# Kernel tuning notes

Hardware: AMD Instinct MI355X
Metric: run time of the kernel (lower is better)

## Reference

```python
import jax, jax.numpy as jnp
import numpy as np

N, K, E = 20000, 4, 320000
IN_DIM, H_IN, D = 1024, 256, 128
GATE_IN = 2 * D + 1  # [h || m || logdeg]
GATE_H = 128         # max(d_out, 32)
TEMP = 0.6
M_CLAMP = 20.0


def _init(key, shape, fan_in):
    return jax.random.normal(key, shape, dtype=jnp.float32) / np.sqrt(fan_in)


def setup_inputs() -> dict:
    key = jax.random.key(0)
    ks = jax.random.split(key, 24)
    inp = {}
    inp['X'] = jax.random.normal(ks[0], (N, IN_DIM), dtype=jnp.float32)
    inp['rows'] = jax.random.randint(ks[1], (K, E), 0, N, dtype=jnp.int32)
    inp['cols'] = jax.random.randint(ks[2], (K, E), 0, N, dtype=jnp.int32)
    inp['mask'] = jnp.ones((N, K), dtype=jnp.float32)
    inp['logdeg'] = jax.random.uniform(ks[3], (N, K), dtype=jnp.float32) * 3.0
    # lin_in: 3-layer MLP 1024 -> 256 -> 256 -> 128, each + ReLU
    inp['W_in0'] = _init(ks[4], (IN_DIM, H_IN), IN_DIM); inp['b_in0'] = jnp.zeros((H_IN,), jnp.float32)
    inp['W_in1'] = _init(ks[5], (H_IN, H_IN), H_IN);     inp['b_in1'] = jnp.zeros((H_IN,), jnp.float32)
    inp['W_in2'] = _init(ks[6], (H_IN, D), H_IN);        inp['b_in2'] = jnp.zeros((D,), jnp.float32)
    # block 0
    inp['Wmsg0'] = _init(ks[7], (D, D), D)
    inp['Wg1_0'] = _init(ks[8], (GATE_IN, GATE_H), GATE_IN); inp['bg1_0'] = jnp.zeros((GATE_H,), jnp.float32)
    inp['Wg2_0'] = _init(ks[9], (GATE_H, 1), GATE_H);        inp['bg2_0'] = jnp.zeros((1,), jnp.float32)
    # block 1
    inp['Wmsg1'] = _init(ks[10], (D, D), D)
    inp['Wg1_1'] = _init(ks[11], (GATE_IN, GATE_H), GATE_IN); inp['bg1_1'] = jnp.zeros((GATE_H,), jnp.float32)
    inp['Wg2_1'] = _init(ks[12], (GATE_H, 1), GATE_H);        inp['bg2_1'] = jnp.zeros((1,), jnp.float32)
    # head
    inp['Wh1'] = _init(ks[13], (D, D), D); inp['bh1'] = jnp.zeros((D,), jnp.float32)
    inp['Wh2'] = _init(ks[14], (D, 1), D); inp['bh2'] = jnp.zeros((1,), jnp.float32)
    return inp


def reference(X, rows, cols, mask, logdeg,
              W_in0, b_in0, W_in1, b_in1, W_in2, b_in2,
              Wmsg0, Wg1_0, bg1_0, Wg2_0, bg2_0,
              Wmsg1, Wg1_1, bg1_1, Wg2_1, bg2_1,
              Wh1, bh1, Wh2, bh2):
    relu = jax.nn.relu
    # input encoder (eval mode: dropout / featdrop are identity)
    H = relu(relu(relu(X @ W_in0 + b_in0) @ W_in1 + b_in1) @ W_in2 + b_in2)

    def pairnorm(x):
        x = x - x.mean(axis=0, keepdims=True)
        mean_norm = jnp.sqrt(jnp.mean(jnp.sum(x * x, axis=1))) + 1e-6
        return x / mean_norm

    def block(H, Wmsg, Wg1, bg1, Wg2, bg2):
        Z = H @ Wmsg  # [N, D]
        def prop(r, c):  # sparse A_k @ Z with binary adjacency: out[r] += Z[c]
            return jax.ops.segment_sum(Z[c], r, num_segments=N)
        M = jnp.transpose(jax.vmap(prop)(rows, cols), (1, 0, 2))  # [N, K, D]
        M = jnp.clip(M, -M_CLAMP, M_CLAMP)
        H_rep = jnp.broadcast_to(H[:, None, :], (N, K, H.shape[1]))
        gate_in = jnp.concatenate([H_rep, M, logdeg[:, :, None]], axis=2)  # [N, K, 2D+1]
        scores = (relu(gate_in @ Wg1 + bg1) @ Wg2 + bg2)[..., 0]  # [N, K]
        alpha = jax.nn.softmax(scores / TEMP, axis=1)
        alpha = alpha * mask
        alpha = alpha / jnp.maximum(alpha.sum(axis=1, keepdims=True), 1e-12)
        alpha = jnp.maximum(alpha, 1e-8)
        alpha = alpha / jnp.maximum(alpha.sum(axis=1, keepdims=True), 1e-12)
        fused = jnp.einsum('nk,nkd->nd', alpha, M)
        return fused, alpha

    fused0, a0 = block(H, Wmsg0, Wg1_0, bg1_0, Wg2_0, bg2_0)
    H = relu(pairnorm(fused0 + H))
    fused1, a1 = block(H, Wmsg1, Wg1_1, bg1_1, Wg2_1, bg2_1)
    H = relu(pairnorm(fused1 + H))

    h = relu(relu(H) @ Wh1 + bh1)
    logits = (h @ Wh2 + bh2)[:, 0]  # [N]
    return logits, jnp.stack([a0, a1], axis=0)
```

## Files before the change

kernel.cpp:

```cpp
#include <hip/hip_runtime.h>
#include <hip/hip_bf16.h>

#define N_NODES 20000
#define KADJ 4
#define NEDGE 320000
#define ETOTAL (KADJ * NEDGE)
#define IN_DIM_ 1024
#define H_IN_ 256
#define DDIM 128
#define GATE_H_ 128
#define TEMP_ 0.6f
#define M_CLAMP_ 20.0f
#define CSR_TOTAL (KADJ * N_NODES)
#define NCOARSE 128
#define QPER (CSR_TOTAL / NCOARSE)
#define ESTRIDE 12288
#define TILE_A 4096
#define BINA_NB ((ETOTAL + TILE_A - 1) / TILE_A)
#define NB_CAST (N_NODES * IN_DIM_ / 8 / 256)
#define NB_TRANS 2560

typedef __attribute__((ext_vector_type(8))) short frag_ab;
typedef __attribute__((ext_vector_type(4))) float frag_cd;
typedef __attribute__((ext_vector_type(8))) unsigned short us8;

__device__ inline unsigned short f2bf(float f) {
    unsigned int u = __float_as_uint(f);
    u += 0x7FFFu + ((u >> 16) & 1);
    return (unsigned short)(u >> 16);
}
__device__ inline float bflo(unsigned int p) { return __uint_as_float(p << 16); }
__device__ inline float bfhi(unsigned int p) { return __uint_as_float(p & 0xffff0000u); }

__device__ __forceinline__ void gld16(const unsigned short* g, unsigned short* l) {
    __builtin_amdgcn_global_load_lds(
        (const __attribute__((address_space(1))) void*)g,
        (__attribute__((address_space(3))) void*)l, 16, 0, 0);
}

#define PIPE_WAIT_NEXT()  asm volatile("s_waitcnt vmcnt(5)" ::: "memory")
#define PIPE_WAIT_LAST()  asm volatile("s_waitcnt vmcnt(0)" ::: "memory")
#define PIPE_BAR()        __builtin_amdgcn_s_barrier()
#define PIPE_FENCE()      __builtin_amdgcn_sched_barrier(0)


struct TD { const float* src; unsigned short* dst; int K; int N; };
struct TD10 { TD d[10]; };

__global__ __launch_bounds__(256) void prep_kernel(
    const float* __restrict__ X, unsigned short* __restrict__ Xb,
    TD10 descs,
    const int* __restrict__ rows, const int* __restrict__ cols,
    int* __restrict__ bcnt, uint2* __restrict__ staging)
{
    __shared__ __align__(16) char sraw[2048 + TILE_A * 8];
    int bid = blockIdx.x;
    int tid = threadIdx.x;

    if (bid < NB_CAST) {
        int i = (bid * 256 + tid) * 8;
        float4 a = *(const float4*)(X + i), b = *(const float4*)(X + i + 4);
        us8 o;
        o[0] = f2bf(a.x); o[1] = f2bf(a.y); o[2] = f2bf(a.z); o[3] = f2bf(a.w);
        o[4] = f2bf(b.x); o[5] = f2bf(b.y); o[6] = f2bf(b.z); o[7] = f2bf(b.w);
        *(us8*)(Xb + i) = o;
        return;
    }
    if (bid < NB_CAST + NB_TRANS) {
        int b2 = bid - NB_CAST;
        TD t = descs.d[b2 >> 8];
        int rem = b2 & 255;
        int n0 = (rem & 7) * 32, k0 = (rem >> 3) * 32;
        if (n0 >= t.N || k0 >= t.K) return;
        float (*tile)[33] = (float(*)[33])sraw;
        int tx = tid & 31, ty4 = (tid >> 5) * 4;
#pragma unroll
        for (int i = 0; i < 4; i++)
            tile[ty4 + i][tx] = t.src[(size_t)(k0 + ty4 + i) * t.N + n0 + tx];
        __syncthreads();
#pragma unroll
        for (int i = 0; i < 4; i++)
            t.dst[(size_t)(n0 + ty4 + i) * t.K + k0 + tx] = f2bf(tile[tx][ty4 + i]);
        return;
    }
    int* hist  = (int*)sraw;
    int* hscan = hist + NCOARSE;
    int* lcur  = hscan + NCOARSE;
    int* gbase = lcur + NCOARSE;
    uint2* pairs = (uint2*)(sraw + 2048);

    int base = (bid - NB_CAST - NB_TRANS) * TILE_A;
    int cnt_t = min(TILE_A, ETOTAL - base);

    for (int i = tid; i < NCOARSE; i += 256) hist[i] = 0;
    __syncthreads();

    unsigned int q[16], c[16];
    bool valid[16];
#pragma unroll
    for (int i = 0; i < 16; i++) {
        int loc = i * 256 + tid;
        valid[i] = loc < cnt_t;
        if (valid[i]) {
            int e = base + loc;
            int k = e / NEDGE;
            unsigned int qq = (unsigned int)(k * N_NODES + rows[e]);
            q[i] = qq;
            c[i] = (unsigned int)cols[e];
            atomicAdd(&hist[qq / QPER], 1);
        }
    }
    __syncthreads();
    if (tid < NCOARSE) hscan[tid] = hist[tid];
    __syncthreads();
    for (int d = 1; d < NCOARSE; d <<= 1) {
        int v = (tid >= d && tid < NCOARSE) ? hscan[tid - d] : 0;
        __syncthreads();
        if (tid < NCOARSE) hscan[tid] += v;
        __syncthreads();
    }
    if (tid < NCOARSE) {
        int ex = hscan[tid] - hist[tid];
        hscan[tid] = ex;
        lcur[tid] = ex;
        gbase[tid] = hist[tid] ? (tid * ESTRIDE + atomicAdd(&bcnt[tid], hist[tid])) : 0;
    }
    __syncthreads();
#pragma unroll
    for (int i = 0; i < 16; i++) {
        if (valid[i]) {
            int b = q[i] / QPER;
            int p = atomicAdd(&lcur[b], 1);
            pairs[p] = make_uint2(q[i], c[i]);
        }
    }
    __syncthreads();
    for (int i = tid; i < cnt_t; i += 256) {
        uint2 pr = pairs[i];
        int b = pr.x / QPER;
        staging[gbase[b] + (i - hscan[b])] = pr;
    }
}

__global__ __launch_bounds__(256) void gemm_async_kernel(
    const unsigned short* __restrict__ A, const unsigned short* __restrict__ Bt,
    const float* __restrict__ bias, float* __restrict__ Cf, unsigned short* __restrict__ Cb,
    int M, int N, int K, int do_relu)
{
    __shared__ unsigned short sA[2][32 * 64];
    __shared__ unsigned short sB[2][128 * 64];
    int tid = threadIdx.x;
    int tileM = blockIdx.y * 32, tileN = blockIdx.x * 128;
    int w = tid >> 6, lane = tid & 63;
    int wr = (w & 1) * 16, wc = (w >> 1) * 64;
    int fm = lane & 15, fq = lane >> 4;
    int crow = lane >> 3;
    int gsw = (lane & 7) ^ crow;

    frag_cd acc[4] = {};

    auto stage = [&](int buf, int k0) {
        {
            int row = w * 8 + crow;
            int ar = min(tileM + row, M - 1);
            gld16(A + (size_t)ar * K + k0 + gsw * 8, &sA[buf][w * 512]);
        }
#pragma unroll
        for (int t = 0; t < 4; t++) {
            int chunk = w * 4 + t;
            int row = chunk * 8 + crow;
            gld16(Bt + (size_t)(tileN + row) * K + k0 + gsw * 8, &sB[buf][chunk * 512]);
        }
    };

    int nt = K >> 6;
    stage(0, 0);
    for (int t = 0; t < nt; t++) {
        int cur = t & 1;
        if (t + 1 < nt) { stage(cur ^ 1, (t + 1) << 6); PIPE_WAIT_NEXT(); }
        else            { PIPE_WAIT_LAST(); }
        PIPE_BAR();
        PIPE_FENCE();
#pragma unroll
        for (int s = 0; s < 2; s++) {
            int sw = ((s * 4 + fq) ^ (fm & 7)) * 8;
            frag_ab af = *(const frag_ab*)&sA[cur][(wr + fm) * 64 + sw];
#pragma unroll
            for (int j = 0; j < 4; j++) {
                frag_ab bf = *(const frag_ab*)&sB[cur][(wc + j * 16 + fm) * 64 + sw];
                acc[j] = __builtin_amdgcn_mfma_f32_16x16x32_bf16(af, bf, acc[j], 0, 0, 0);
            }
        }
        PIPE_FENCE();
        PIPE_BAR();
    }
    int row = tileM + wr + fq * 4;
#pragma unroll
    for (int r = 0; r < 4; r++) {
        if (row + r < M) {
#pragma unroll
            for (int j = 0; j < 4; j++) {
                int col = tileN + wc + j * 16 + fm;
                float v = acc[j][r];
                if (bias) v += bias[col];
                if (do_relu) v = fmaxf(v, 0.f);
                if (Cf) Cf[(size_t)(row + r) * N + col] = v;
                if (Cb) Cb[(size_t)(row + r) * N + col] = f2bf(v);
            }
        }
    }
}

__global__ __launch_bounds__(256) void zg_gemm_kernel(
    const unsigned short* __restrict__ A, const unsigned short* __restrict__ Bt,
    const float* __restrict__ bg1, unsigned short* __restrict__ Zb,
    float* __restrict__ GH, int M)
{
    __shared__ unsigned short sA[2][32 * 64];
    __shared__ unsigned short sB[2][128 * 64];
    int tid = threadIdx.x;
    int tileM = blockIdx.y * 32, tileN = blockIdx.x * 128;
    int w = tid >> 6, lane = tid & 63;
    int wr = (w & 1) * 16, wc = (w >> 1) * 64;
    int fm = lane & 15, fq = lane >> 4;
    int crow = lane >> 3;
    int gsw = (lane & 7) ^ crow;

    frag_cd acc[4] = {};

    auto stage = [&](int buf, int k0) {
        {
            int row = w * 8 + crow;
            int ar = min(tileM + row, M - 1);
            gld16(A + (size_t)ar * DDIM + k0 + gsw * 8, &sA[buf][w * 512]);
        }
#pragma unroll
        for (int t = 0; t < 4; t++) {
            int chunk = w * 4 + t;
            int row = chunk * 8 + crow;
            gld16(Bt + (size_t)(tileN + row) * DDIM + k0 + gsw * 8, &sB[buf][chunk * 512]);
        }
    };

    stage(0, 0);
#pragma unroll
    for (int t = 0; t < 2; t++) {
        int cur = t & 1;
        if (t == 0) { stage(1, 64); PIPE_WAIT_NEXT(); }
        else        { PIPE_WAIT_LAST(); }
        PIPE_BAR();
        PIPE_FENCE();
#pragma unroll
        for (int s = 0; s < 2; s++) {
            int sw = ((s * 4 + fq) ^ (fm & 7)) * 8;
            frag_ab af = *(const frag_ab*)&sA[cur][(wr + fm) * 64 + sw];
#pragma unroll
            for (int j = 0; j < 4; j++) {
                frag_ab bf = *(const frag_ab*)&sB[cur][(wc + j * 16 + fm) * 64 + sw];
                acc[j] = __builtin_amdgcn_mfma_f32_16x16x32_bf16(af, bf, acc[j], 0, 0, 0);
            }
        }
        PIPE_FENCE();
        PIPE_BAR();
    }
    int isZ = (blockIdx.x == 0);
    int row = tileM + wr + fq * 4;
#pragma unroll
    for (int r = 0; r < 4; r++) {
        if (row + r < M) {
#pragma unroll
            for (int j = 0; j < 4; j++) {
                int col = wc + j * 16 + fm;
                float v = acc[j][r];
                if (isZ) Zb[(size_t)(row + r) * DDIM + col] = f2bf(v);
                else     GH[(size_t)(row + r) * GATE_H_ + col] = v + bg1[col];
            }
        }
    }
}

__global__ __launch_bounds__(256) void head_gemm_kernel(
    const unsigned short* __restrict__ A, const unsigned short* __restrict__ Bt,
    const float* __restrict__ bh1, const float* __restrict__ Wh2,
    const float* __restrict__ bh2, float* __restrict__ logits, int M)
{
    __shared__ unsigned short sA[2][32 * 64];
    __shared__ unsigned short sB[2][128 * 64];
    __shared__ float sred[2][32];
    int tid = threadIdx.x;
    int tileM = blockIdx.x * 32;
    int w = tid >> 6, lane = tid & 63;
    int wr = (w & 1) * 16, wc = (w >> 1) * 64;
    int fm = lane & 15, fq = lane >> 4;
    int crow = lane >> 3;
    int gsw = (lane & 7) ^ crow;

    frag_cd acc[4] = {};

    auto stage = [&](int buf, int k0) {
        {
            int row = w * 8 + crow;
            int ar = min(tileM + row, M - 1);
            gld16(A + (size_t)ar * DDIM + k0 + gsw * 8, &sA[buf][w * 512]);
        }
#pragma unroll
        for (int t = 0; t < 4; t++) {
            int chunk = w * 4 + t;
            int row = chunk * 8 + crow;
            gld16(Bt + (size_t)row * DDIM + k0 + gsw * 8, &sB[buf][chunk * 512]);
        }
    };

    stage(0, 0);
#pragma unroll
    for (int t = 0; t < 2; t++) {
        int cur = t & 1;
        if (t == 0) { stage(1, 64); PIPE_WAIT_NEXT(); }
        else        { PIPE_WAIT_LAST(); }
        PIPE_BAR();
        PIPE_FENCE();
#pragma unroll
        for (int s = 0; s < 2; s++) {
            int sw = ((s * 4 + fq) ^ (fm & 7)) * 8;
            frag_ab af = *(const frag_ab*)&sA[cur][(wr + fm) * 64 + sw];
#pragma unroll
            for (int j = 0; j < 4; j++) {
                frag_ab bf = *(const frag_ab*)&sB[cur][(wc + j * 16 + fm) * 64 + sw];
                acc[j] = __builtin_amdgcn_mfma_f32_16x16x32_bf16(af, bf, acc[j], 0, 0, 0);
            }
        }
        PIPE_FENCE();
        PIPE_BAR();
    }
    float wv[4], bh[4];
#pragma unroll
    for (int j = 0; j < 4; j++) {
        int c = wc + j * 16 + fm;
        wv[j] = Wh2[c];
        bh[j] = bh1[c];
    }
    float part[4];
#pragma unroll
    for (int r = 0; r < 4; r++) {
        float p = 0.f;
#pragma unroll
        for (int j = 0; j < 4; j++) {
            float v = fmaxf(acc[j][r] + bh[j], 0.f);
            p += v * wv[j];
        }
        part[r] = p;
    }
#pragma unroll
    for (int m = 1; m < 16; m <<= 1)
#pragma unroll
        for (int r = 0; r < 4; r++)
            part[r] += __shfl_xor(part[r], m, 64);
    if (fm == 0) {
#pragma unroll
        for (int r = 0; r < 4; r++)
            sred[w >> 1][wr + fq * 4 + r] = part[r];
    }
    __syncthreads();
    if (tid < 32 && tileM + tid < M)
        logits[tileM + tid] = sred[0][tid] + sred[1][tid] + bh2[0];
}

__global__ __launch_bounds__(256) void gate_fuse_kernel(
    const unsigned short* __restrict__ Mb, const unsigned short* __restrict__ Bt,
    const float* __restrict__ GH, const float* __restrict__ logdeg,
    const float* __restrict__ wld, const float* __restrict__ Wg2,
    const float* __restrict__ bg2, const float* __restrict__ mask,
    const float* __restrict__ H, float* __restrict__ Y,
    float* __restrict__ alpha_out, float* __restrict__ red)
{
    __shared__ unsigned short sA[2][32 * 64];
    __shared__ unsigned short sB[2][128 * 64];
    __shared__ float sred[2][32];
    __shared__ float sc_al[64];
    __shared__ float sx[256], sy[256], sqs[256];
    int tid = threadIdx.x;
    int tile0 = blockIdx.x * 32;
    int node0 = blockIdx.x * 8;
    int w = tid >> 6, lane = tid & 63;
    int wr = (w & 1) * 16, wc = (w >> 1) * 64;
    int fm = lane & 15, fq = lane >> 4;
    int crow = lane >> 3;
    int gsw = (lane & 7) ^ crow;

    frag_cd acc[4] = {};

    auto stage = [&](int buf, int k0) {
        {
            int row = w * 8 + crow;
            gld16(Mb + (size_t)(tile0 + row) * DDIM + k0 + gsw * 8, &sA[buf][w * 512]);
        }
#pragma unroll
        for (int t = 0; t < 4; t++) {
            int chunk = w * 4 + t;
            int row = chunk * 8 + crow;
            gld16(Bt + (size_t)row * DDIM + k0 + gsw * 8, &sB[buf][chunk * 512]);
        }
    };

    stage(0, 0);
#pragma unroll
    for (int t = 0; t < 2; t++) {
        int cur = t & 1;
        if (t == 0) { stage(1, 64); PIPE_WAIT_NEXT(); }
        else        { PIPE_WAIT_LAST(); }
        PIPE_BAR();
        PIPE_FENCE();
#pragma unroll
        for (int s = 0; s < 2; s++) {
            int sw = ((s * 4 + fq) ^ (fm & 7)) * 8;
            frag_ab af = *(const frag_ab*)&sA[cur][(wr + fm) * 64 + sw];
#pragma unroll
            for (int j = 0; j < 4; j++) {
                frag_ab bf = *(const frag_ab*)&sB[cur][(wc + j * 16 + fm) * 64 + sw];
                acc[j] = __builtin_amdgcn_mfma_f32_16x16x32_bf16(af, bf, acc[j], 0, 0, 0);
            }
        }
        PIPE_FENCE();
        PIPE_BAR();
    }
    float wg2v[4], wldv[4];
#pragma unroll
    for (int j = 0; j < 4; j++) {
        int c = wc + j * 16 + fm;
        wg2v[j] = Wg2[c];
        wldv[j] = wld[c];
    }
    float part[4];
#pragma unroll
    for (int r = 0; r < 4; r++) {
        int q = tile0 + wr + fq * 4 + r;
        int n = q >> 2;
        float ld = logdeg[q];
        float p = 0.f;
#pragma unroll
        for (int j = 0; j < 4; j++) {
            int c = wc + j * 16 + fm;
            float v = acc[j][r] + GH[(size_t)n * GATE_H_ + c] + ld * wldv[j];
            p += fmaxf(v, 0.f) * wg2v[j];
        }
        part[r] = p;
    }
#pragma unroll
    for (int m = 1; m < 16; m <<= 1)
#pragma unroll
        for (int r = 0; r < 4; r++)
            part[r] += __shfl_xor(part[r], m, 64);
    if (fm == 0) {
#pragma unroll
        for (int r = 0; r < 4; r++)
            sred[w >> 1][wr + fq * 4 + r] = part[r];
    }
    __syncthreads();
    if (tid < 32) sc_al[tid] = sred[0][tid] + sred[1][tid] + bg2[0];
    __syncthreads();
    if (tid < 8) {
        int n = node0 + tid;
        float a[KADJ];
        float mx = -1e30f;
#pragma unroll
        for (int k = 0; k < KADJ; k++) {
            a[k] = sc_al[tid * 4 + k] * (1.0f / TEMP_);
            mx = fmaxf(mx, a[k]);
        }
        float sum = 0.f;
#pragma unroll
        for (int k = 0; k < KADJ; k++) { a[k] = expf(a[k] - mx); sum += a[k]; }
#pragma unroll
        for (int k = 0; k < KADJ; k++) a[k] = (a[k] / sum) * mask[(size_t)n * KADJ + k];
        float s2 = 0.f;
#pragma unroll
        for (int k = 0; k < KADJ; k++) s2 += a[k];
        float inv = 1.f / fmaxf(s2, 1e-12f);
#pragma unroll
        for (int k = 0; k < KADJ; k++) a[k] = fmaxf(a[k] * inv, 1e-8f);
        s2 = 0.f;
#pragma unroll
        for (int k = 0; k < KADJ; k++) s2 += a[k];
        inv = 1.f / fmaxf(s2, 1e-12f);
#pragma unroll
        for (int k = 0; k < KADJ; k++) sc_al[32 + tid * 4 + k] = a[k] * inv;
    }
    __syncthreads();
    if (tid < 32) alpha_out[tile0 + tid] = sc_al[32 + tid];
    float csx = 0.f, csy = 0.f, sq = 0.f;
    int j = tid & 63, dd = j * 2;
#pragma unroll
    for (int it = 0; it < 2; it++) {
        int nl = (tid >> 6) + it * 4;
        int n = node0 + nl;
        const float* alp = &sc_al[32 + nl * 4];
        float2 h = *(const float2*)(H + (size_t)n * DDIM + dd);
        float yx = h.x, yy = h.y;
#pragma unroll
        for (int k = 0; k < KADJ; k++) {
            unsigned int u = *(const unsigned int*)(Mb + ((size_t)n * KADJ + k) * DDIM + dd);
            yx += alp[k] * bflo(u);
            yy += alp[k] * bfhi(u);
        }
        *(float2*)(Y + (size_t)n * DDIM + dd) = make_float2(yx, yy);
        csx += yx; csy += yy;
        sq += yx * yx + yy * yy;
    }
    sx[tid] = csx; sy[tid] = csy; sqs[tid] = sq;
    __syncthreads();
    int st = (blockIdx.x & 7) * 132;
    if (tid < 64) {
        float ax = sx[tid] + sx[tid + 64] + sx[tid + 128] + sx[tid + 192];
        float ay = sy[tid] + sy[tid + 64] + sy[tid + 128] + sy[tid + 192];
        atomicAdd(&red[st + tid * 2], ax);
        atomicAdd(&red[st + tid * 2 + 1], ay);
    }
    for (int s = 128; s > 0; s >>= 1) {
        if (tid < s) sqs[tid] += sqs[tid + s];
        __syncthreads();
    }
    if (tid == 0) atomicAdd(&red[st + 128], sqs[0]);
}

__global__ __launch_bounds__(256) void binB2_kernel(
    const uint2* __restrict__ staging, const int* __restrict__ bcnt,
    int* __restrict__ offs, int* __restrict__ ends, int* __restrict__ edst)
{
    __shared__ int cntS[QPER], sofs[QPER], lcur[QPER];
    __shared__ int psum[256];
    int tid = threadIdx.x, b = blockIdx.x;
    int q0 = b * QPER, base = b * ESTRIDE;
    int fill = bcnt[b];
    for (int i = tid; i < QPER; i += 256) cntS[i] = 0;
    __syncthreads();
    for (int i = tid; i < fill; i += 256)
        atomicAdd(&cntS[staging[base + i].x - q0], 1);
    __syncthreads();
    const int CH = 3;
    int lo = tid * CH, hi = min(lo + CH, QPER);
    int s = 0;
    for (int i = lo; i < hi; i++) s += cntS[i];
    psum[tid] = s;
    __syncthreads();
    for (int d = 1; d < 256; d <<= 1) {
        int v = (tid >= d) ? psum[tid - d] : 0;
        __syncthreads();
        psum[tid] += v;
        __syncthreads();
    }
    int run = (tid == 0) ? 0 : psum[tid - 1];
    for (int i = lo; i < hi; i++) {
        sofs[i] = run;
        lcur[i] = run;
        run += cntS[i];
    }
    __syncthreads();
    for (int i = tid; i < QPER; i += 256) {
        offs[q0 + i] = base + sofs[i];
        ends[q0 + i] = base + sofs[i] + cntS[i];
    }
    for (int i = tid; i < fill; i += 256) {
        uint2 p = staging[base + i];
        int pos = atomicAdd(&lcur[p.x - q0], 1);
        edst[base + pos] = (int)p.y;
    }
}

__global__ __launch_bounds__(256) void gather_kernel(
    const int* __restrict__ offs, const int* __restrict__ ends,
    const int* __restrict__ edst,
    const unsigned short* __restrict__ Zb, unsigned short* __restrict__ Mb)
{
    int q = blockIdx.x * 4 + (threadIdx.x >> 6);
    int lane = threadIdx.x & 63;
    int qw = lane >> 4;
    int l = lane & 15;
    int k = q / N_NODES;
    int r = q - k * N_NODES;
    int start = offs[q];
    int end = ends[q];

    float a0 = 0.f, a1 = 0.f, a2 = 0.f, a3 = 0.f;
    float a4 = 0.f, a5 = 0.f, a6 = 0.f, a7 = 0.f;

#define ACC8(P) {                                  \
        a0 += bflo(P.x); a1 += bfhi(P.x);          \
        a2 += bflo(P.y); a3 += bfhi(P.y);          \
        a4 += bflo(P.z); a5 += bfhi(P.z);          \
        a6 += bflo(P.w); a7 += bfhi(P.w); }

    int i = start + qw;
    for (; i + 12 < end; i += 16) {
        int c0 = edst[i], c1 = edst[i + 4], c2 = edst[i + 8], c3 = edst[i + 12];
        uint4 p0 = *(const uint4*)(Zb + (size_t)c0 * DDIM + l * 8);
        uint4 p1 = *(const uint4*)(Zb + (size_t)c1 * DDIM + l * 8);
        uint4 p2 = *(const uint4*)(Zb + (size_t)c2 * DDIM + l * 8);
        uint4 p3 = *(const uint4*)(Zb + (size_t)c3 * DDIM + l * 8);
        ACC8(p0); ACC8(p1); ACC8(p2); ACC8(p3);
    }
    for (; i + 4 < end; i += 8) {
        int c0 = edst[i], c1 = edst[i + 4];
        uint4 p0 = *(const uint4*)(Zb + (size_t)c0 * DDIM + l * 8);
        uint4 p1 = *(const uint4*)(Zb + (size_t)c1 * DDIM + l * 8);
        ACC8(p0); ACC8(p1);
    }
    if (i < end) {
        int c0 = edst[i];
        uint4 p0 = *(const uint4*)(Zb + (size_t)c0 * DDIM + l * 8);
        ACC8(p0);
    }
#undef ACC8

#define QRED(x) { x += __shfl_xor(x, 16, 64); x += __shfl_xor(x, 32, 64); }
    QRED(a0) QRED(a1) QRED(a2) QRED(a3) QRED(a4) QRED(a5) QRED(a6) QRED(a7)
#undef QRED

#define CLIP(v) fminf(fmaxf(v, -M_CLAMP_), M_CLAMP_)
    unsigned int w0 = (unsigned int)f2bf(CLIP(a0)) | ((unsigned int)f2bf(CLIP(a1)) << 16);
    unsigned int w1 = (unsigned int)f2bf(CLIP(a2)) | ((unsigned int)f2bf(CLIP(a3)) << 16);
    unsigned int w2 = (unsigned int)f2bf(CLIP(a4)) | ((unsigned int)f2bf(CLIP(a5)) << 16);
    unsigned int w3 = (unsigned int)f2bf(CLIP(a6)) | ((unsigned int)f2bf(CLIP(a7)) << 16);
#undef CLIP
    if (qw == 0) {
        uint4 o = make_uint4(w0, w1, w2, w3);
        *(uint4*)(Mb + ((size_t)r * KADJ + k) * DDIM + l * 8) = o;
    }
}

__global__ __launch_bounds__(256) void pairnorm_kernel(
    const float* __restrict__ Y, const float* __restrict__ red,
    float* __restrict__ Hout, unsigned short* __restrict__ Hb, int N)
{
    int tid = threadIdx.x;
    int d = tid & 127;
    float invN = 1.0f / (float)N;
    float s = 0.f, rq = 0.f;
#pragma unroll
    for (int st = 0; st < 8; st++) {
        s += red[st * 132 + d];
        rq += red[st * 132 + 128];
    }
    float mu = s * invN;
    __shared__ float smu2[128];
    if (tid < 128) smu2[tid] = mu * mu;
    __syncthreads();
    for (int t = 64; t > 0; t >>= 1) {
        if (tid < t) smu2[tid] += smu2[tid + t];
        __syncthreads();
    }
    float summu2 = smu2[0];
    float var = rq * invN - summu2;
    float norm = sqrtf(fmaxf(var, 0.f)) + 1e-6f;
    float inv = 1.0f / norm;
    int n = blockIdx.x * 2 + (tid >> 7);
    if (n < N) {
        float v = (Y[(size_t)n * DDIM + d] - mu) * inv;
        v = fmaxf(v, 0.f);
        Hout[(size_t)n * DDIM + d] = v;
        Hb[(size_t)n * DDIM + d] = f2bf(v);
    }
}

extern "C" void kernel_launch(void* const* d_in, const int* in_sizes, int n_in,
                              void* d_out, int out_size, void* d_ws, size_t ws_size,
                              hipStream_t stream)
{
    const float* X      = (const float*)d_in[0];
    const int*   rows   = (const int*)d_in[1];
    const int*   cols   = (const int*)d_in[2];
    const float* mask   = (const float*)d_in[3];
    const float* logdeg = (const float*)d_in[4];
    const float* W_in0  = (const float*)d_in[5];
    const float* b_in0  = (const float*)d_in[6];
    const float* W_in1  = (const float*)d_in[7];
    const float* b_in1  = (const float*)d_in[8];
    const float* W_in2  = (const float*)d_in[9];
    const float* b_in2  = (const float*)d_in[10];
    const float* Wmsg[2] = {(const float*)d_in[11], (const float*)d_in[16]};
    const float* Wg1[2]  = {(const float*)d_in[12], (const float*)d_in[17]};
    const float* bg1[2]  = {(const float*)d_in[13], (const float*)d_in[18]};
    const float* Wg2[2]  = {(const float*)d_in[14], (const float*)d_in[19]};
    const float* bg2[2]  = {(const float*)d_in[15], (const float*)d_in[20]};
    const float* Wh1 = (const float*)d_in[21];
    const float* bh1 = (const float*)d_in[22];
    const float* Wh2 = (const float*)d_in[23];
    const float* bh2 = (const float*)d_in[24];

    float* ws = (float*)d_ws;
    unsigned short* Xb  = (unsigned short*)ws;
    unsigned short* Mb  = (unsigned short*)ws;
    float* Ybuf  = ws + 5120000;
    float* GH    = ws + 7680000;
    uint2* staging = (uint2*)(ws + 10240000);
    unsigned short* H0b = (unsigned short*)(ws + 10240000);
    unsigned short* H1b = (unsigned short*)(ws + 12800000);
    unsigned short* Zb  = (unsigned short*)(ws + 12800000);
    float* H     = ws + 15360000;
    unsigned short* Hb = (unsigned short*)(ws + 17920000);
    int*   bcnt  = (int*)(ws + 19200000);
    float* red   = ws + 19200128;
    int*   offs   = (int*)(ws + 19280000);
    int*   ends   = (int*)(ws + 19360000);
    int*   edst   = (int*)(ws + 19440000);
    unsigned short* w0t  = (unsigned short*)(ws + 21013248);
    unsigned short* w1t  = (unsigned short*)(ws + 21144320);
    unsigned short* w2t  = (unsigned short*)(ws + 21177088);
    unsigned short* wzg[2]  = {(unsigned short*)(ws + 21193472), (unsigned short*)(ws + 21209856)};
    unsigned short* wgmt[2] = {(unsigned short*)(ws + 21226240), (unsigned short*)(ws + 21234432)};
    unsigned short* wh1t = (unsigned short*)(ws + 21242624);
    float* logits = (float*)d_out;
    float* alpha_out = (float*)d_out + N_NODES;

    dim3 blk(256);
    int gM32 = (N_NODES + 31) / 32;

    (void)hipMemsetAsync(bcnt, 0, (128 + 2 * 8 * 132) * sizeof(float), stream);

    TD10 descs;
    descs.d[0] = {W_in0, w0t, IN_DIM_, H_IN_};
    descs.d[1] = {W_in1, w1t, H_IN_, H_IN_};
    descs.d[2] = {W_in2, w2t, H_IN_, DDIM};
    descs.d[3] = {Wmsg[0], wzg[0], DDIM, DDIM};
    descs.d[4] = {Wg1[0], wzg[0] + DDIM * DDIM, DDIM, GATE_H_};
    descs.d[5] = {Wmsg[1], wzg[1], DDIM, DDIM};
    descs.d[6] = {Wg1[1], wzg[1] + DDIM * DDIM, DDIM, GATE_H_};
    descs.d[7] = {Wg1[0] + DDIM * GATE_H_, wgmt[0], DDIM, GATE_H_};
    descs.d[8] = {Wg1[1] + DDIM * GATE_H_, wgmt[1], DDIM, GATE_H_};
    descs.d[9] = {Wh1, wh1t, DDIM, DDIM};
    prep_kernel<<<NB_CAST + NB_TRANS + BINA_NB, blk, 0, stream>>>(
        X, Xb, descs, rows, cols, bcnt, staging);
    binB2_kernel<<<NCOARSE, blk, 0, stream>>>(staging, bcnt, offs, ends, edst);

    gemm_async_kernel<<<dim3(2, gM32), blk, 0, stream>>>(Xb, w0t, b_in0, nullptr, H0b, N_NODES, H_IN_, IN_DIM_, 1);
    gemm_async_kernel<<<dim3(2, gM32), blk, 0, stream>>>(H0b, w1t, b_in1, nullptr, H1b, N_NODES, H_IN_, H_IN_, 1);
    gemm_async_kernel<<<dim3(1, gM32), blk, 0, stream>>>(H1b, w2t, b_in2, H, Hb, N_NODES, DDIM, H_IN_, 1);

    for (int b = 0; b < 2; b++) {
        zg_gemm_kernel<<<dim3(2, gM32), blk, 0, stream>>>(Hb, wzg[b], bg1[b], Zb, GH, N_NODES);
        gather_kernel<<<CSR_TOTAL / 4, blk, 0, stream>>>(offs, ends, edst, Zb, Mb);
        float* alph = alpha_out + (size_t)b * N_NODES * KADJ;
        gate_fuse_kernel<<<CSR_TOTAL / 32, blk, 0, stream>>>(
            Mb, wgmt[b], GH, logdeg, Wg1[b] + 256 * GATE_H_, Wg2[b], bg2[b],
            mask, H, Ybuf, alph, red + b * 8 * 132);
        pairnorm_kernel<<<(N_NODES + 1) / 2, blk, 0, stream>>>(Ybuf, red + b * 8 * 132, H, Hb, N_NODES);
    }

    head_gemm_kernel<<<gM32, blk, 0, stream>>>(Hb, wh1t, bh1, Wh2, bh2, logits, N_NODES);
}
```

Before: 456.7 us.

## Fuse neighbor gather into gate kernel and merge CSR binning into first GEMM

The sparse neighbor aggregation now runs inside gate_fuse_kernel: each wave gathers and sums Z rows for its 8 queries and writes the clipped bf16 results straight into the swizzled shared A tile. This removes the separate gather kernel and the write and re-read of the Mb buffer. The second CSR binning pass is appended as extra blocks of the first input GEMM launch, saving a launch and letting the two overlap. The staging buffer moves so it no longer aliases the GEMM output, and prep block order is rearranged. The risk is that each wave now walks its 8 gathers one after another, so latency hiding may drop compared with the standalone gather grid.

```diff
diff --git a/kernel.cpp b/kernel.cpp
--- a/kernel.cpp
+++ b/kernel.cpp
@@ -57,8 +57,8 @@
     int bid = blockIdx.x;
     int tid = threadIdx.x;
 
-    if (bid < NB_CAST) {
-        int i = (bid * 256 + tid) * 8;
+    if (bid >= BINA_NB + NB_TRANS) {
+        int i = ((bid - BINA_NB - NB_TRANS) * 256 + tid) * 8;
         float4 a = *(const float4*)(X + i), b = *(const float4*)(X + i + 4);
         us8 o;
         o[0] = f2bf(a.x); o[1] = f2bf(a.y); o[2] = f2bf(a.z); o[3] = f2bf(a.w);
@@ -66,8 +66,8 @@
         *(us8*)(Xb + i) = o;
         return;
     }
-    if (bid < NB_CAST + NB_TRANS) {
-        int b2 = bid - NB_CAST;
+    if (bid >= BINA_NB) {
+        int b2 = bid - BINA_NB;
         TD t = descs.d[b2 >> 8];
         int rem = b2 & 255;
         int n0 = (rem & 7) * 32, k0 = (rem >> 3) * 32;
@@ -89,7 +89,7 @@
     int* gbase = lcur + NCOARSE;
     uint2* pairs = (uint2*)(sraw + 2048);
 
-    int base = (bid - NB_CAST - NB_TRANS) * TILE_A;
+    int base = bid * TILE_A;
     int cnt_t = min(TILE_A, ETOTAL - base);
 
     for (int i = tid; i < NCOARSE; i += 256) hist[i] = 0;
@@ -139,6 +139,121 @@
         uint2 pr = pairs[i];
         int b = pr.x / QPER;
         staging[gbase[b] + (i - hscan[b])] = pr;
+    }
+}
+
+__global__ __launch_bounds__(256) void gemm1_binb_kernel(
+    const unsigned short* __restrict__ A, const unsigned short* __restrict__ Bt,
+    const float* __restrict__ bias, unsigned short* __restrict__ Cb,
+    int M, int N, int K,
+    const uint2* __restrict__ staging, const int* __restrict__ bcnt,
+    int* __restrict__ offs, int* __restrict__ ends, int* __restrict__ edst)
+{
+    __shared__ __align__(16) char smem[40960];
+    int tid = threadIdx.x;
+    int bid = blockIdx.x;
+    const int GEMM_NB = 2 * 625;
+
+    if (bid < GEMM_NB) {
+        unsigned short* sA0 = (unsigned short*)smem;
+        unsigned short* sB0 = (unsigned short*)(smem + 8192);
+        int tileM = (bid >> 1) * 32, tileN = (bid & 1) * 128;
+        int w = tid >> 6, lane = tid & 63;
+        int wr = (w & 1) * 16, wc = (w >> 1) * 64;
+        int fm = lane & 15, fq = lane >> 4;
+        int crow = lane >> 3;
+        int gsw = (lane & 7) ^ crow;
+
+        frag_cd acc[4] = {};
+
+        auto stage = [&](int buf, int k0) {
+            {
+                int row = w * 8 + crow;
+                int ar = min(tileM + row, M - 1);
+                gld16(A + (size_t)ar * K + k0 + gsw * 8, sA0 + buf * 2048 + w * 512);
+            }
+#pragma unroll
+            for (int t = 0; t < 4; t++) {
+                int chunk = w * 4 + t;
+                int row = chunk * 8 + crow;
+                gld16(Bt + (size_t)(tileN + row) * K + k0 + gsw * 8, sB0 + buf * 8192 + chunk * 512);
+            }
+        };
+
+        int nt = K >> 6;
+        stage(0, 0);
+        for (int t = 0; t < nt; t++) {
+            int cur = t & 1;
+            if (t + 1 < nt) { stage(cur ^ 1, (t + 1) << 6); PIPE_WAIT_NEXT(); }
+            else            { PIPE_WAIT_LAST(); }
+            PIPE_BAR();
+            PIPE_FENCE();
+#pragma unroll
+            for (int s = 0; s < 2; s++) {
+                int sw = ((s * 4 + fq) ^ (fm & 7)) * 8;
+                frag_ab af = *(const frag_ab*)(sA0 + cur * 2048 + (wr + fm) * 64 + sw);
+#pragma unroll
+                for (int j = 0; j < 4; j++) {
+                    frag_ab bf = *(const frag_ab*)(sB0 + cur * 8192 + (wc + j * 16 + fm) * 64 + sw);
+                    acc[j] = __builtin_amdgcn_mfma_f32_16x16x32_bf16(af, bf, acc[j], 0, 0, 0);
+                }
+            }
+            PIPE_FENCE();
+            PIPE_BAR();
+        }
+        int row = tileM + wr + fq * 4;
+#pragma unroll
+        for (int r = 0; r < 4; r++) {
+            if (row + r < M) {
+#pragma unroll
+                for (int j = 0; j < 4; j++) {
+                    int col = tileN + wc + j * 16 + fm;
+                    float v = fmaxf(acc[j][r] + bias[col], 0.f);
+                    Cb[(size_t)(row + r) * N + col] = f2bf(v);
+                }
+            }
+        }
+        return;
+    }
+    int* cntS = (int*)smem;
+    int* sofs = cntS + QPER;
+    int* lcur = sofs + QPER;
+    int* psum = lcur + QPER;
+    int b = bid - GEMM_NB;
+    int q0 = b * QPER, base = b * ESTRIDE;
+    int fill = bcnt[b];
+    for (int i = tid; i < QPER; i += 256) cntS[i] = 0;
+    __syncthreads();
+    for (int i = tid; i < fill; i += 256)
+        atomicAdd(&cntS[staging[base + i].x - q0], 1);
+    __syncthreads();
+    const int CH = 3;
+    int lo = tid * CH, hi = min(lo + CH, QPER);
+    int s = 0;
+    for (int i = lo; i < hi; i++) s += cntS[i];
+    psum[tid] = s;
+    __syncthreads();
+    for (int d = 1; d < 256; d <<= 1) {
+        int v = (tid >= d) ? psum[tid - d] : 0;
+        __syncthreads();
+        psum[tid] += v;
+        __syncthreads();
+    }
+    int run = (tid == 0) ? 0 : psum[tid - 1];
+    for (int i = lo; i < hi; i++) {
+        sofs[i] = run;
+        lcur[i] = run;
+        run += cntS[i];
+    }
+    __syncthreads();
+    for (int i = tid; i < QPER; i += 256) {
+        offs[q0 + i] = base + sofs[i];
+        ends[q0 + i] = base + sofs[i] + cntS[i];
+    }
+    for (int i = tid; i < fill; i += 256) {
+        uint2 p = staging[base + i];
+        int pos = atomicAdd(&lcur[p.x - q0], 1);
+        edst[base + pos] = (int)p.y;
     }
 }
 
@@ -366,15 +481,17 @@
 }
 
 __global__ __launch_bounds__(256) void gate_fuse_kernel(
-    const unsigned short* __restrict__ Mb, const unsigned short* __restrict__ Bt,
+    const int* __restrict__ offs, const int* __restrict__ ends,
+    const int* __restrict__ edst, const unsigned short* __restrict__ Zb,
+    const unsigned short* __restrict__ Bt,
     const float* __restrict__ GH, const float* __restrict__ logdeg,
     const float* __restrict__ wld, const float* __restrict__ Wg2,
     const float* __restrict__ bg2, const float* __restrict__ mask,
     const float* __restrict__ H, float* __restrict__ Y,
     float* __restrict__ alpha_out, float* __restrict__ red)
 {
-    __shared__ unsigned short sA[2][32 * 64];
-    __shared__ unsigned short sB[2][128 * 64];
+    __shared__ __align__(16) unsigned short sA[2][32 * 64];
+    __shared__ __align__(16) unsigned short sB[2][128 * 64];
     __shared__ float sred[2][32];
     __shared__ float sc_al[64];
     __shared__ float sx[256], sy[256], sqs[256];
@@ -387,41 +504,81 @@
     int crow = lane >> 3;
     int gsw = (lane & 7) ^ crow;
 
+#pragma unroll
+    for (int t = 0; t < 4; t++) {
+        int chunk = w * 4 + t;
+        int row = chunk * 8 + crow;
+        gld16(Bt + (size_t)row * DDIM + 0  + gsw * 8, &sB[0][chunk * 512]);
+        gld16(Bt + (size_t)row * DDIM + 64 + gsw * 8, &sB[1][chunk * 512]);
+    }
+
+    int qw = lane >> 4;
+    int l = lane & 15;
+    for (int qi = 0; qi < 8; qi++) {
+        int lq = w * 8 + qi;
+        int qp = tile0 + lq;
+        int r = qp >> 2, kk = qp & 3;
+        int qc = kk * N_NODES + r;
+        int start = offs[qc], end = ends[qc];
+
+        float a0 = 0.f, a1 = 0.f, a2 = 0.f, a3 = 0.f;
+        float a4 = 0.f, a5 = 0.f, a6 = 0.f, a7 = 0.f;
+#define ACC8(P) {                                  \
+        a0 += bflo(P.x); a1 += bfhi(P.x);          \
+        a2 += bflo(P.y); a3 += bfhi(P.y);          \
+        a4 += bflo(P.z); a5 += bfhi(P.z);          \
+        a6 += bflo(P.w); a7 += bfhi(P.w); }
+        int i = start + qw;
+        for (; i + 12 < end; i += 16) {
+            int c0 = edst[i], c1 = edst[i + 4], c2 = edst[i + 8], c3 = edst[i + 12];
+            uint4 p0 = *(const uint4*)(Zb + (size_t)c0 * DDIM + l * 8);
+            uint4 p1 = *(const uint4*)(Zb + (size_t)c1 * DDIM + l * 8);
+            uint4 p2 = *(const uint4*)(Zb + (size_t)c2 * DDIM + l * 8);
+            uint4 p3 = *(const uint4*)(Zb + (size_t)c3 * DDIM + l * 8);
+            ACC8(p0); ACC8(p1); ACC8(p2); ACC8(p3);
+        }
+        for (; i + 4 < end; i += 8) {
+            int c0 = edst[i], c1 = edst[i + 4];
+            uint4 p0 = *(const uint4*)(Zb + (size_t)c0 * DDIM + l * 8);
+            uint4 p1 = *(const uint4*)(Zb + (size_t)c1 * DDIM + l * 8);
+            ACC8(p0); ACC8(p1);
+        }
+        if (i < end) {
+            int c0 = edst[i];
+            uint4 p0 = *(const uint4*)(Zb + (size_t)c0 * DDIM + l * 8);
+            ACC8(p0);
+        }
+#undef ACC8
+#define QRED(x) { x += __shfl_xor(x, 16, 64); x += __shfl_xor(x, 32, 64); }
+        QRED(a0) QRED(a1) QRED(a2) QRED(a3) QRED(a4) QRED(a5) QRED(a6) QRED(a7)
+#undef QRED
+        if (qw == 0) {
+#define CLIP(v) fminf(fmaxf(v, -M_CLAMP_), M_CLAMP_)
+            unsigned int w0 = (unsigned int)f2bf(CLIP(a0)) | ((unsigned int)f2bf(CLIP(a1)) << 16);
+            unsigned int w1 = (unsigned int)f2bf(CLIP(a2)) | ((unsigned int)f2bf(CLIP(a3)) << 16);
+            unsigned int w2 = (unsigned int)f2bf(CLIP(a4)) | ((unsigned int)f2bf(CLIP(a5)) << 16);
+            unsigned int w3 = (unsigned int)f2bf(CLIP(a6)) | ((unsigned int)f2bf(CLIP(a7)) << 16);
+#undef CLIP
+            int buf = l >> 3, gg = l & 7, cr = lq & 7;
+            int soff = w * 512 + (cr * 8 + (gg ^ cr)) * 8;
+            *(uint4*)&sA[buf][soff] = make_uint4(w0, w1, w2, w3);
+        }
+    }
+    __syncthreads();
+
     frag_cd acc[4] = {};
-
-    auto stage = [&](int buf, int k0) {
-        {
-            int row = w * 8 + crow;
-            gld16(Mb + (size_t)(tile0 + row) * DDIM + k0 + gsw * 8, &sA[buf][w * 512]);
-        }
-#pragma unroll
-        for (int t = 0; t < 4; t++) {
-            int chunk = w * 4 + t;
-            int row = chunk * 8 + crow;
-            gld16(Bt + (size_t)row * DDIM + k0 + gsw * 8, &sB[buf][chunk * 512]);
-        }
-    };
-
-    stage(0, 0);
-#pragma unroll
-    for (int t = 0; t < 2; t++) {
-        int cur = t & 1;
-        if (t == 0) { stage(1, 64); PIPE_WAIT_NEXT(); }
-        else        { PIPE_WAIT_LAST(); }
-        PIPE_BAR();
-        PIPE_FENCE();
+#pragma unroll
+    for (int tkt = 0; tkt < 2; tkt++) {
 #pragma unroll
         for (int s = 0; s < 2; s++) {
             int sw = ((s * 4 + fq) ^ (fm & 7)) * 8;
-            frag_ab af = *(const frag_ab*)&sA[cur][(wr + fm) * 64 + sw];
+            frag_ab af = *(const frag_ab*)&sA[tkt][(wr + fm) * 64 + sw];
 #pragma unroll
             for (int j = 0; j < 4; j++) {
-                frag_ab bf = *(const frag_ab*)&sB[cur][(wc + j * 16 + fm) * 64 + sw];
+                frag_ab bf = *(const frag_ab*)&sB[tkt][(wc + j * 16 + fm) * 64 + sw];
                 acc[j] = __builtin_amdgcn_mfma_f32_16x16x32_bf16(af, bf, acc[j], 0, 0, 0);
             }
         }
-        PIPE_FENCE();
-        PIPE_BAR();
     }
     float wg2v[4], wldv[4];
 #pragma unroll
@@ -489,6 +646,7 @@
     if (tid < 32) alpha_out[tile0 + tid] = sc_al[32 + tid];
     float csx = 0.f, csy = 0.f, sq = 0.f;
     int j = tid & 63, dd = j * 2;
+    int g = dd >> 3, mbuf = g >> 3, gg2 = g & 7, din = dd & 7;
 #pragma unroll
     for (int it = 0; it < 2; it++) {
         int nl = (tid >> 6) + it * 4;
@@ -498,7 +656,9 @@
         float yx = h.x, yy = h.y;
 #pragma unroll
         for (int k = 0; k < KADJ; k++) {
-            unsigned int u = *(const unsigned int*)(Mb + ((size_t)n * KADJ + k) * DDIM + dd);
+            int row = nl * 4 + k;
+            int soff = (row >> 3) * 512 + ((row & 7) * 8 + (gg2 ^ (row & 7))) * 8 + din;
+            unsigned int u = *(const unsigned int*)&sA[mbuf][soff];
             yx += alp[k] * bflo(u);
             yy += alp[k] * bfhi(u);
         }
@@ -520,111 +680,6 @@
         __syncthreads();
     }
     if (tid == 0) atomicAdd(&red[st + 128], sqs[0]);
-}
-
-__global__ __launch_bounds__(256) void binB2_kernel(
-    const uint2* __restrict__ staging, const int* __restrict__ bcnt,
-    int* __restrict__ offs, int* __restrict__ ends, int* __restrict__ edst)
-{
-    __shared__ int cntS[QPER], sofs[QPER], lcur[QPER];
-    __shared__ int psum[256];
-    int tid = threadIdx.x, b = blockIdx.x;
-    int q0 = b * QPER, base = b * ESTRIDE;
-    int fill = bcnt[b];
-    for (int i = tid; i < QPER; i += 256) cntS[i] = 0;
-    __syncthreads();
-    for (int i = tid; i < fill; i += 256)
-        atomicAdd(&cntS[staging[base + i].x - q0], 1);
-    __syncthreads();
-    const int CH = 3;
-    int lo = tid * CH, hi = min(lo + CH, QPER);
-    int s = 0;
-    for (int i = lo; i < hi; i++) s += cntS[i];
-    psum[tid] = s;
-    __syncthreads();
-    for (int d = 1; d < 256; d <<= 1) {
-        int v = (tid >= d) ? psum[tid - d] : 0;
-        __syncthreads();
-        psum[tid] += v;
-        __syncthreads();
-    }
-    int run = (tid == 0) ? 0 : psum[tid - 1];
-    for (int i = lo; i < hi; i++) {
-        sofs[i] = run;
-        lcur[i] = run;
-        run += cntS[i];
-    }
-    __syncthreads();
-    for (int i = tid; i < QPER; i += 256) {
-        offs[q0 + i] = base + sofs[i];
-        ends[q0 + i] = base + sofs[i] + cntS[i];
-    }
-    for (int i = tid; i < fill; i += 256) {
-        uint2 p = staging[base + i];
-        int pos = atomicAdd(&lcur[p.x - q0], 1);
-        edst[base + pos] = (int)p.y;
-    }
-}
-
-__global__ __launch_bounds__(256) void gather_kernel(
-    const int* __restrict__ offs, const int* __restrict__ ends,
-    const int* __restrict__ edst,
-    const unsigned short* __restrict__ Zb, unsigned short* __restrict__ Mb)
-{
-    int q = blockIdx.x * 4 + (threadIdx.x >> 6);
-    int lane = threadIdx.x & 63;
-    int qw = lane >> 4;
-    int l = lane & 15;
-    int k = q / N_NODES;
-    int r = q - k * N_NODES;
-    int start = offs[q];
-    int end = ends[q];
-
-    float a0 = 0.f, a1 = 0.f, a2 = 0.f, a3 = 0.f;
-    float a4 = 0.f, a5 = 0.f, a6 = 0.f, a7 = 0.f;
-
-#define ACC8(P) {                                  \
-        a0 += bflo(P.x); a1 += bfhi(P.x);          \
-        a2 += bflo(P.y); a3 += bfhi(P.y);          \
-        a4 += bflo(P.z); a5 += bfhi(P.z);          \
-        a6 += bflo(P.w); a7 += bfhi(P.w); }
-
-    int i = start + qw;
-    for (; i + 12 < end; i += 16) {
-        int c0 = edst[i], c1 = edst[i + 4], c2 = edst[i + 8], c3 = edst[i + 12];
-        uint4 p0 = *(const uint4*)(Zb + (size_t)c0 * DDIM + l * 8);
-        uint4 p1 = *(const uint4*)(Zb + (size_t)c1 * DDIM + l * 8);
-        uint4 p2 = *(const uint4*)(Zb + (size_t)c2 * DDIM + l * 8);
-        uint4 p3 = *(const uint4*)(Zb + (size_t)c3 * DDIM + l * 8);
-        ACC8(p0); ACC8(p1); ACC8(p2); ACC8(p3);
-    }
-    for (; i + 4 < end; i += 8) {
-        int c0 = edst[i], c1 = edst[i + 4];
-        uint4 p0 = *(const uint4*)(Zb + (size_t)c0 * DDIM + l * 8);
-        uint4 p1 = *(const uint4*)(Zb + (size_t)c1 * DDIM + l * 8);
-        ACC8(p0); ACC8(p1);
-    }
-    if (i < end) {
-        int c0 = edst[i];
-        uint4 p0 = *(const uint4*)(Zb + (size_t)c0 * DDIM + l * 8);
-        ACC8(p0);
-    }
-#undef ACC8
-
-#define QRED(x) { x += __shfl_xor(x, 16, 64); x += __shfl_xor(x, 32, 64); }
-    QRED(a0) QRED(a1) QRED(a2) QRED(a3) QRED(a4) QRED(a5) QRED(a6) QRED(a7)
-#undef QRED
-
-#define CLIP(v) fminf(fmaxf(v, -M_CLAMP_), M_CLAMP_)
-    unsigned int w0 = (unsigned int)f2bf(CLIP(a0)) | ((unsigned int)f2bf(CLIP(a1)) << 16);
-    unsigned int w1 = (unsigned int)f2bf(CLIP(a2)) | ((unsigned int)f2bf(CLIP(a3)) << 16);
-    unsigned int w2 = (unsigned int)f2bf(CLIP(a4)) | ((unsigned int)f2bf(CLIP(a5)) << 16);
-    unsigned int w3 = (unsigned int)f2bf(CLIP(a6)) | ((unsigned int)f2bf(CLIP(a7)) << 16);
-#undef CLIP
-    if (qw == 0) {
-        uint4 o = make_uint4(w0, w1, w2, w3);
-        *(uint4*)(Mb + ((size_t)r * KADJ + k) * DDIM + l * 8) = o;
-    }
 }
 
 __global__ __launch_bounds__(256) void pairnorm_kernel(
@@ -688,13 +743,12 @@
 
     float* ws = (float*)d_ws;
     unsigned short* Xb  = (unsigned short*)ws;
-    unsigned short* Mb  = (unsigned short*)ws;
     float* Ybuf  = ws + 5120000;
     float* GH    = ws + 7680000;
-    uint2* staging = (uint2*)(ws + 10240000);
     unsigned short* H0b = (unsigned short*)(ws + 10240000);
     unsigned short* H1b = (unsigned short*)(ws + 12800000);
     unsigned short* Zb  = (unsigned short*)(ws + 12800000);
+    uint2* staging = (uint2*)(ws + 15360000);
     float* H     = ws + 15360000;
     unsigned short* Hb = (unsigned short*)(ws + 17920000);
     int*   bcnt  = (int*)(ws + 19200000);
@@ -727,21 +781,22 @@
     descs.d[7] = {Wg1[0] + DDIM * GATE_H_, wgmt[0], DDIM, GATE_H_};
     descs.d[8] = {Wg1[1] + DDIM * GATE_H_, wgmt[1], DDIM, GATE_H_};
     descs.d[9] = {Wh1, wh1t, DDIM, DDIM};
-    prep_kernel<<<NB_CAST + NB_TRANS + BINA_NB, blk, 0, stream>>>(
+    prep_kernel<<<BINA_NB + NB_TRANS + NB_CAST, blk, 0, stream>>>(
         X, Xb, descs, rows, cols, bcnt, staging);
-    binB2_kernel<<<NCOARSE, blk, 0, stream>>>(staging, bcnt, offs, ends, edst);
-
-    gemm_async_kernel<<<dim3(2, gM32), blk, 0, stream>>>(Xb, w0t, b_in0, nullptr, H0b, N_NODES, H_IN_, IN_DIM_, 1);
+
+    gemm1_binb_kernel<<<2 * gM32 + NCOARSE, blk, 0, stream>>>(
+        Xb, w0t, b_in0, H0b, N_NODES, H_IN_, IN_DIM_,
+        staging, bcnt, offs, ends, edst);
+
     gemm_async_kernel<<<dim3(2, gM32), blk, 0, stream>>>(H0b, w1t, b_in1, nullptr, H1b, N_NODES, H_IN_, H_IN_, 1);
     gemm_async_kernel<<<dim3(1, gM32), blk, 0, stream>>>(H1b, w2t, b_in2, H, Hb, N_NODES, DDIM, H_IN_, 1);
 
     for (int b = 0; b < 2; b++) {
         zg_gemm_kernel<<<dim3(2, gM32), blk, 0, stream>>>(Hb, wzg[b], bg1[b], Zb, GH, N_NODES);
-        gather_kernel<<<CSR_TOTAL / 4, blk, 0, stream>>>(offs, ends, edst, Zb, Mb);
         float* alph = alpha_out + (size_t)b * N_NODES * KADJ;
         gate_fuse_kernel<<<CSR_TOTAL / 32, blk, 0, stream>>>(
-            Mb, wgmt[b], GH, logdeg, Wg1[b] + 256 * GATE_H_, Wg2[b], bg2[b],
-            mask, H, Ybuf, alph, red + b * 8 * 132);
+            offs, ends, edst, Zb, wgmt[b], GH, logdeg, Wg1[b] + 256 * GATE_H_,
+            Wg2[b], bg2[b], mask, H, Ybuf, alph, red + b * 8 * 132);
         pairnorm_kernel<<<(N_NODES + 1) / 2, blk, 0, stream>>>(Ybuf, red + b * 8 * 132, H, Hb, N_NODES);
     }
 
```

Measured after the change: 469.9 us. +2.9%, slower.
